# Kernel tuning notes

Measured on AMD Instinct MI355X. Metric: run time of the kernel, lower is better.

## Reference

```python
import jax, jax.numpy as jnp
import numpy as np

INV_SQRT2 = 0.7071067811865476  # ResidualLayer scale in GemNet
SILU_SCALE = 1.0 / 0.6          # ScaledSiLU scale factor


def scaled_silu(x):
    return jax.nn.silu(x) * SILU_SCALE


def setup_inputs() -> dict:
    key = jax.random.key(0)
    ks = jax.random.split(key, 9)
    E, A, D, NB = 200000, 10000, 256, 5  # edges, atoms, emb_size_edge, int_blocks+1

    def w(k, shape):
        fan_in = shape[0]
        return jax.random.normal(k, shape, jnp.float32) * (2.0 / fan_in) ** 0.5

    return {
        "x_cat": jax.random.normal(ks[0], (E, D * NB), jnp.float32),
        "edge_vec": jax.random.normal(ks[1], (E, 3), jnp.float32),
        "edge_idx": jax.random.randint(ks[2], (E,), 0, A),
        "W_in": w(ks[3], (D * NB, D)),
        "W_r1a": w(ks[4], (D, D)),
        "W_r1b": w(ks[5], (D, D)),
        "W_r2a": w(ks[6], (D, D)),
        "W_r2b": w(ks[7], (D, D)),
        "W_out": w(ks[8], (D, 1)),
        "n_atoms": A,
    }


def reference(x_cat, edge_vec, edge_idx, W_in, W_r1a, W_r1b, W_r2a, W_r2b, W_out, n_atoms):
    # out_mlp_F: Dense(in->emb) + 2 residual layers (all Dense are bias-free + ScaledSiLU)
    x = scaled_silu(x_cat @ W_in)                                   # [E, D]
    x = (x + scaled_silu(scaled_silu(x @ W_r1a) @ W_r1b)) * INV_SQRT2
    x = (x + scaled_silu(scaled_silu(x @ W_r2a) @ W_r2b)) * INV_SQRT2
    # out_forces: Dense(D -> 1, bias=False, no activation)
    F_st = x @ W_out                                                # [E, 1]
    # F_st_vec = F_st[:, :, None] * edge_vec[:, None, :] -> squeeze the size-1 dim
    F_vec = F_st * edge_vec                                         # [E, 3]
    # scatter_add over target atom index
    forces = jax.ops.segment_sum(F_vec, edge_idx, num_segments=n_atoms)  # [A, 3]
    return forces
```

## Files before the change

kernel.cpp:

```cpp
#include <hip/hip_runtime.h>

typedef __attribute__((ext_vector_type(4))) float f32x4;
typedef __attribute__((ext_vector_type(8))) __bf16 bf16x8;
typedef __attribute__((ext_vector_type(8))) unsigned short us8;
typedef unsigned short u16;

#define SSILU_SCALE (1.0f / 0.6f)
#define INV_SQRT2 0.70710678118654752f

__device__ __forceinline__ u16 f2bf(float f) {
    __bf16 h = (__bf16)f;
    return __builtin_bit_cast(u16, h);
}
__device__ __forceinline__ float bf2f(u16 h) {
    union { unsigned int u; float f; } v; v.u = ((unsigned int)h) << 16;
    return v.f;
}
__device__ __forceinline__ float ssilu(float x) {
    float e = __expf(-x);
    float s = __builtin_amdgcn_rcpf(1.0f + e);
    return x * s * SSILU_SCALE;
}

__global__ __launch_bounds__(256) void prep_kernel(
    const float* __restrict__ Win, const float* __restrict__ W1a,
    const float* __restrict__ W1b, const float* __restrict__ W2a,
    const float* __restrict__ W2b, u16* __restrict__ WinF,
    u16* __restrict__ Wfrag, float* __restrict__ out, int outN) {
    int i = blockIdx.x * 256 + threadIdx.x;
    if (i < 327680) {
        int e = i & 7, lane = (i >> 3) & 63, n = (i >> 9) & 3;
        int kk = (i >> 11) & 1, w = (i >> 12) & 3, kt = i >> 14;
        int lo = lane & 15, hi = lane >> 4;
        int k = kt * 64 + kk * 32 + hi * 8 + e;
        int col = w * 64 + n * 16 + lo;
        WinF[i] = f2bf(Win[k * 256 + col]);
        return;
    }
    int j = i - 327680;
    if (j < 262144) {
        int g = j >> 16, r = j & 65535;
        int chunk = r >> 9, within = r & 511;
        int lane = within >> 3, e = within & 7;
        int w = chunk >> 5, kk = (chunk >> 2) & 7, n = chunk & 3;
        int lo = lane & 15, hi = lane >> 4;
        int col = w * 64 + n * 16 + lo;
        int k = kk * 32 + hi * 8 + e;
        const float* W = (g == 0) ? W1a : (g == 1) ? W1b : (g == 2) ? W2a : W2b;
        Wfrag[j] = f2bf(W[k * 256 + col]);
        return;
    }
    int z = j - 262144;
    if (z < outN) out[z] = 0.0f;
}

__global__ __launch_bounds__(256, 2) void fused_kernel(
    const float* __restrict__ A, const u16* __restrict__ WinF,
    const u16* __restrict__ Wfrag, const float* __restrict__ Wout,
    const float* __restrict__ evec, const int* __restrict__ eidx,
    float* __restrict__ out) {
    __shared__ u16 xb[64 * 256];
    __shared__ u16 tb[64 * 256];
    __shared__ float fpart[4][64];
    const int t = threadIdx.x, w = t >> 6, l = t & 63;
    const int lo = l & 15, hi = l >> 4;
    const int swz = (lo & 7) << 4;
    const long rowbase = (long)blockIdx.x * 64;
    char* xbB = (char*)xb;
    char* tbB = (char*)tb;
    char* As0 = tbB;
    char* As1 = tbB + 16384;

    f32x4 acc[4][4];
#pragma unroll
    for (int m = 0; m < 4; m++)
#pragma unroll
        for (int n = 0; n < 4; n++) acc[m][n] = (f32x4){0.f, 0.f, 0.f, 0.f};

    float4 va[4][2];
    auto LOADA = [&](int kb) {
#pragma unroll
        for (int c = 0; c < 4; ++c) {
            int idx = t + c * 256;
            int r = idx >> 4, k8 = (idx & 15) * 8;
            const float* s = A + (rowbase + r) * 1280 + kb + k8;
            va[c][0] = *(const float4*)s;
            va[c][1] = *(const float4*)(s + 4);
        }
    };
    auto WRITEA = [&](char* dst) {
#pragma unroll
        for (int c = 0; c < 4; ++c) {
            int idx = t + c * 256;
            int r = idx >> 4, k8 = (idx & 15) * 8;
            us8 p;
            p[0] = f2bf(va[c][0].x); p[1] = f2bf(va[c][0].y);
            p[2] = f2bf(va[c][0].z); p[3] = f2bf(va[c][0].w);
            p[4] = f2bf(va[c][1].x); p[5] = f2bf(va[c][1].y);
            p[6] = f2bf(va[c][1].z); p[7] = f2bf(va[c][1].w);
            *(us8*)(dst + r * 256 + ((k8 * 2) ^ ((r & 7) << 4))) = p;
        }
    };
    const u16* WinFw = WinF + w * 4096 + l * 8;
    auto LOADB = [&](int kt, bf16x8 (&b)[8]) {
        const u16* base = WinFw + kt * 16384;
#pragma unroll
        for (int kkL = 0; kkL < 2; ++kkL)
#pragma unroll
            for (int n = 0; n < 4; ++n)
                b[kkL * 4 + n] = __builtin_bit_cast(bf16x8,
                    *(const us8*)(base + kkL * 2048 + n * 512));
    };
    auto MFMA_HALF = [&](const char* AB, int half, const bf16x8 (&b)[8]) {
#pragma unroll
        for (int kkL = 0; kkL < 2; ++kkL) {
            int kbyte = (half * 2 + kkL) * 64 + hi * 16;
            bf16x8 af[4];
#pragma unroll
            for (int m = 0; m < 4; m++) {
                int r = m * 16 + lo;
                af[m] = __builtin_bit_cast(bf16x8,
                    *(const us8*)(AB + r * 256 + (kbyte ^ swz)));
            }
#pragma unroll
            for (int m = 0; m < 4; m++)
#pragma unroll
                for (int n = 0; n < 4; n++)
                    acc[m][n] = __builtin_amdgcn_mfma_f32_16x16x32_bf16(
                        af[m], b[kkL * 4 + n], acc[m][n], 0, 0, 0);
        }
    };
    auto FENCE = [&]() {
        asm volatile("s_waitcnt lgkmcnt(0)" ::: "memory");
        __builtin_amdgcn_sched_barrier(0);
        __builtin_amdgcn_s_barrier();
    };

    {
        bf16x8 bc[8], bn[8];

        LOADA(0);
        WRITEA(As0);
        LOADB(0, bc);
        LOADA(128);
        FENCE();

        auto STEP = [&](int s, const char* AScur, char* ASnxt) {
            const bool more = (s < 9);
            LOADB(2 * s + 1, bn);
            __builtin_amdgcn_sched_barrier(0);
            MFMA_HALF(AScur, 0, bc);
            if (more) LOADB(2 * s + 2, bc);
            MFMA_HALF(AScur, 1, bn);
            if (more) WRITEA(ASnxt);
            if (s <= 7) LOADA((s + 2) * 128);
            FENCE();
        };

        for (int i = 0; i < 5; ++i) {
            STEP(2 * i,     As0, As1);
            STEP(2 * i + 1, As1, As0);
        }
    }

#pragma unroll
    for (int m = 0; m < 4; m++)
#pragma unroll
        for (int n = 0; n < 4; n++)
#pragma unroll
            for (int j = 0; j < 4; j++) {
                int r = m * 16 + hi * 4 + j;
                int cc = w * 64 + n * 16 + lo;
                *(u16*)(xbB + r * 512 + ((cc * 2) ^ ((r & 7) << 4))) =
                    f2bf(ssilu(acc[m][n][j]));
            }

    const u16* Wfw = Wfrag + w * 16384;
    bf16x8 b0[4], b1[4], b2[4];

    auto LW = [&](const u16* Wg, int kk, bf16x8 (&b)[4]) {
        const u16* base = Wg + kk * 2048 + l * 8;
#pragma unroll
        for (int n = 0; n < 4; ++n)
            b[n] = __builtin_bit_cast(bf16x8, *(const us8*)(base + n * 512));
    };
    auto GEMM = [&](const char* AB, const u16* Wg) {
#pragma unroll
        for (int m = 0; m < 4; m++)
#pragma unroll
            for (int n = 0; n < 4; n++) acc[m][n] = (f32x4){0.f, 0.f, 0.f, 0.f};
#pragma unroll
        for (int kk = 0; kk < 8; ++kk) {
            if (kk < 6) {
                const int s = (kk + 2) % 3;
                if (s == 0)      LW(Wg, kk + 2, b0);
                else if (s == 1) LW(Wg, kk + 2, b1);
                else             LW(Wg, kk + 2, b2);
            }
            int kbyte = kk * 64 + hi * 16;
            bf16x8 af[4];
#pragma unroll
            for (int m = 0; m < 4; m++) {
                int r = m * 16 + lo;
                af[m] = __builtin_bit_cast(bf16x8,
                    *(const us8*)(AB + r * 512 + (kbyte ^ ((r & 7) << 4))));
            }
            const bf16x8 (&bu)[4] = (kk % 3 == 0) ? b0 : (kk % 3 == 1) ? b1 : b2;
#pragma unroll
            for (int m = 0; m < 4; m++)
#pragma unroll
                for (int n = 0; n < 4; n++)
                    acc[m][n] = __builtin_amdgcn_mfma_f32_16x16x32_bf16(
                        af[m], bu[n], acc[m][n], 0, 0, 0);
        }
    };

    LW(Wfw + 0 * 65536, 0, b0);
    LW(Wfw + 0 * 65536, 1, b1);
    FENCE();
    GEMM(xbB, Wfw + 0 * 65536);
#pragma unroll
    for (int m = 0; m < 4; m++)
#pragma unroll
        for (int n = 0; n < 4; n++)
#pragma unroll
            for (int j = 0; j < 4; j++) {
                int r = m * 16 + hi * 4 + j;
                int cc = w * 64 + n * 16 + lo;
                *(u16*)(tbB + r * 512 + ((cc * 2) ^ ((r & 7) << 4))) =
                    f2bf(ssilu(acc[m][n][j]));
            }
    LW(Wfw + 1 * 65536, 0, b0);
    LW(Wfw + 1 * 65536, 1, b1);
    FENCE();

    GEMM(tbB, Wfw + 1 * 65536);
#pragma unroll
    for (int m = 0; m < 4; m++)
#pragma unroll
        for (int n = 0; n < 4; n++)
#pragma unroll
            for (int j = 0; j < 4; j++) {
                int r = m * 16 + hi * 4 + j;
                int cc = w * 64 + n * 16 + lo;
                char* p = xbB + r * 512 + ((cc * 2) ^ ((r & 7) << 4));
                float xn = (bf2f(*(u16*)p) + ssilu(acc[m][n][j])) * INV_SQRT2;
                *(u16*)p = f2bf(xn);
            }
    LW(Wfw + 2 * 65536, 0, b0);
    LW(Wfw + 2 * 65536, 1, b1);
    FENCE();

    GEMM(xbB, Wfw + 2 * 65536);
#pragma unroll
    for (int m = 0; m < 4; m++)
#pragma unroll
        for (int n = 0; n < 4; n++)
#pragma unroll
            for (int j = 0; j < 4; j++) {
                int r = m * 16 + hi * 4 + j;
                int cc = w * 64 + n * 16 + lo;
                *(u16*)(tbB + r * 512 + ((cc * 2) ^ ((r & 7) << 4))) =
                    f2bf(ssilu(acc[m][n][j]));
            }
    LW(Wfw + 3 * 65536, 0, b0);
    LW(Wfw + 3 * 65536, 1, b1);
    FENCE();

    GEMM(tbB, Wfw + 3 * 65536);
    float wo[4];
#pragma unroll
    for (int n = 0; n < 4; n++) wo[n] = Wout[w * 64 + n * 16 + lo];

    float part[4][4];
#pragma unroll
    for (int m = 0; m < 4; m++)
#pragma unroll
        for (int j = 0; j < 4; j++) part[m][j] = 0.f;
#pragma unroll
    for (int m = 0; m < 4; m++)
#pragma unroll
        for (int n = 0; n < 4; n++)
#pragma unroll
            for (int j = 0; j < 4; j++) {
                int r = m * 16 + hi * 4 + j;
                int cc = w * 64 + n * 16 + lo;
                const char* p = xbB + r * 512 + ((cc * 2) ^ ((r & 7) << 4));
                float xf = (bf2f(*(const u16*)p) + ssilu(acc[m][n][j])) * INV_SQRT2;
                part[m][j] += xf * wo[n];
            }
#pragma unroll
    for (int m = 0; m < 4; m++)
#pragma unroll
        for (int j = 0; j < 4; j++) {
            float v = part[m][j];
            v += __shfl_xor(v, 1);
            v += __shfl_xor(v, 2);
            v += __shfl_xor(v, 4);
            v += __shfl_xor(v, 8);
            if (lo == 0) fpart[w][m * 16 + hi * 4 + j] = v;
        }
    __syncthreads();

    if (t < 64) {
        int r = t;
        float F = fpart[0][r] + fpart[1][r] + fpart[2][r] + fpart[3][r];
        long e = rowbase + r;
        float vx = evec[e * 3 + 0], vy = evec[e * 3 + 1], vz = evec[e * 3 + 2];
        int a = eidx[e];
        atomicAdd(&out[a * 3 + 0], F * vx);
        atomicAdd(&out[a * 3 + 1], F * vy);
        atomicAdd(&out[a * 3 + 2], F * vz);
    }
}

extern "C" void kernel_launch(void* const* d_in, const int* in_sizes, int n_in,
                              void* d_out, int out_size, void* d_ws, size_t ws_size,
                              hipStream_t stream) {
    const float* x_cat = (const float*)d_in[0];
    const float* evec  = (const float*)d_in[1];
    const int*   eidx  = (const int*)d_in[2];
    const float* Win   = (const float*)d_in[3];
    const float* W1a   = (const float*)d_in[4];
    const float* W1b   = (const float*)d_in[5];
    const float* W2a   = (const float*)d_in[6];
    const float* W2b   = (const float*)d_in[7];
    const float* Wout  = (const float*)d_in[8];
    float* out = (float*)d_out;
    const int E = in_sizes[1] / 3;

    u16* WinF  = (u16*)d_ws;
    u16* Wfrag = WinF + 327680;

    int prepN = 327680 + 262144 + out_size;
    prep_kernel<<<(prepN + 255) / 256, 256, 0, stream>>>(
        Win, W1a, W1b, W2a, W2b, WinF, Wfrag, out, out_size);
    fused_kernel<<<E / 64, 256, 0, stream>>>(
        x_cat, WinF, Wfrag, Wout, evec, eidx, out);
}
```

Baseline: 383.8 us.

## Warp-specialize fused MLP into persistent producer/consumer blocks

Replaces the one-tile-per-block kernel with a persistent grid of 256 blocks of 512 threads. Half the threads run the input GEMM (x_cat @ W_in) for tile s into a double-buffered activation buffer, while the other half run the four residual GEMMs and the scatter for tile s-1. The two roles stay in lockstep by issuing matching barrier counts. The goal is to overlap the bandwidth-bound input streaming with the compute-bound residual MLP. In exchange, each role gets half the waves, the A staging tile shrinks to K=64, and correctness depends on the barrier counts matching exactly.

```diff
diff --git a/kernel.cpp b/kernel.cpp
--- a/kernel.cpp
+++ b/kernel.cpp
@@ -54,263 +54,277 @@
     if (z < outN) out[z] = 0.0f;
 }
 
-__global__ __launch_bounds__(256, 2) void fused_kernel(
+__global__ __launch_bounds__(512, 1) void fused_pc(
     const float* __restrict__ A, const u16* __restrict__ WinF,
     const u16* __restrict__ Wfrag, const float* __restrict__ Wout,
     const float* __restrict__ evec, const int* __restrict__ eidx,
-    float* __restrict__ out) {
-    __shared__ u16 xb[64 * 256];
+    float* __restrict__ out, int ntiles) {
+    __shared__ u16 xb[2][64 * 256];
+    __shared__ u16 As[2][64 * 64];
     __shared__ u16 tb[64 * 256];
     __shared__ float fpart[4][64];
-    const int t = threadIdx.x, w = t >> 6, l = t & 63;
+    const int tid = threadIdx.x;
+    const int role = __builtin_amdgcn_readfirstlane(tid >> 8);
+    const int t = tid & 255;
+    const int w = t >> 6, l = t & 63;
     const int lo = l & 15, hi = l >> 4;
     const int swz = (lo & 7) << 4;
-    const long rowbase = (long)blockIdx.x * 64;
-    char* xbB = (char*)xb;
-    char* tbB = (char*)tb;
-    char* As0 = tbB;
-    char* As1 = tbB + 16384;
-
-    f32x4 acc[4][4];
-#pragma unroll
-    for (int m = 0; m < 4; m++)
-#pragma unroll
-        for (int n = 0; n < 4; n++) acc[m][n] = (f32x4){0.f, 0.f, 0.f, 0.f};
-
-    float4 va[4][2];
-    auto LOADA = [&](int kb) {
-#pragma unroll
-        for (int c = 0; c < 4; ++c) {
-            int idx = t + c * 256;
-            int r = idx >> 4, k8 = (idx & 15) * 8;
-            const float* s = A + (rowbase + r) * 1280 + kb + k8;
-            va[c][0] = *(const float4*)s;
-            va[c][1] = *(const float4*)(s + 4);
-        }
-    };
-    auto WRITEA = [&](char* dst) {
-#pragma unroll
-        for (int c = 0; c < 4; ++c) {
-            int idx = t + c * 256;
-            int r = idx >> 4, k8 = (idx & 15) * 8;
-            us8 p;
-            p[0] = f2bf(va[c][0].x); p[1] = f2bf(va[c][0].y);
-            p[2] = f2bf(va[c][0].z); p[3] = f2bf(va[c][0].w);
-            p[4] = f2bf(va[c][1].x); p[5] = f2bf(va[c][1].y);
-            p[6] = f2bf(va[c][1].z); p[7] = f2bf(va[c][1].w);
-            *(us8*)(dst + r * 256 + ((k8 * 2) ^ ((r & 7) << 4))) = p;
-        }
-    };
-    const u16* WinFw = WinF + w * 4096 + l * 8;
-    auto LOADB = [&](int kt, bf16x8 (&b)[8]) {
-        const u16* base = WinFw + kt * 16384;
-#pragma unroll
-        for (int kkL = 0; kkL < 2; ++kkL)
-#pragma unroll
-            for (int n = 0; n < 4; ++n)
-                b[kkL * 4 + n] = __builtin_bit_cast(bf16x8,
-                    *(const us8*)(base + kkL * 2048 + n * 512));
-    };
-    auto MFMA_HALF = [&](const char* AB, int half, const bf16x8 (&b)[8]) {
-#pragma unroll
-        for (int kkL = 0; kkL < 2; ++kkL) {
-            int kbyte = (half * 2 + kkL) * 64 + hi * 16;
-            bf16x8 af[4];
-#pragma unroll
-            for (int m = 0; m < 4; m++) {
-                int r = m * 16 + lo;
-                af[m] = __builtin_bit_cast(bf16x8,
-                    *(const us8*)(AB + r * 256 + (kbyte ^ swz)));
-            }
-#pragma unroll
-            for (int m = 0; m < 4; m++)
-#pragma unroll
-                for (int n = 0; n < 4; n++)
-                    acc[m][n] = __builtin_amdgcn_mfma_f32_16x16x32_bf16(
-                        af[m], b[kkL * 4 + n], acc[m][n], 0, 0, 0);
-        }
-    };
-    auto FENCE = [&]() {
+    const int bid = blockIdx.x;
+    const int NT = (ntiles - bid + 255) / 256;
+
+    auto BAR = []() { __builtin_amdgcn_s_barrier(); };
+    auto FENCE = []() {
         asm volatile("s_waitcnt lgkmcnt(0)" ::: "memory");
         __builtin_amdgcn_sched_barrier(0);
         __builtin_amdgcn_s_barrier();
     };
 
-    {
-        bf16x8 bc[8], bn[8];
-
-        LOADA(0);
-        WRITEA(As0);
-        LOADB(0, bc);
-        LOADA(128);
-        FENCE();
-
-        auto STEP = [&](int s, const char* AScur, char* ASnxt) {
-            const bool more = (s < 9);
-            LOADB(2 * s + 1, bn);
-            __builtin_amdgcn_sched_barrier(0);
-            MFMA_HALF(AScur, 0, bc);
-            if (more) LOADB(2 * s + 2, bc);
-            MFMA_HALF(AScur, 1, bn);
-            if (more) WRITEA(ASnxt);
-            if (s <= 7) LOADA((s + 2) * 128);
-            FENCE();
-        };
-
-        for (int i = 0; i < 5; ++i) {
-            STEP(2 * i,     As0, As1);
-            STEP(2 * i + 1, As1, As0);
+    if (role == 0) {
+        char* As0 = (char*)As[0];
+        char* As1 = (char*)As[1];
+        const u16* WinFw = WinF + w * 4096 + l * 8;
+        for (int s = 0; s <= NT; ++s) {
+            if (s >= NT) {
+                for (int k = 0; k < 22; ++k) BAR();
+                continue;
+            }
+            const long rowbase = (long)(bid + 256 * s) * 64;
+            char* xbp = (char*)xb[s & 1];
+
+            f32x4 acc[4][4];
+#pragma unroll
+            for (int m = 0; m < 4; m++)
+#pragma unroll
+                for (int n = 0; n < 4; n++) acc[m][n] = (f32x4){0.f, 0.f, 0.f, 0.f};
+
+            float4 va[2][2];
+            auto LOADA = [&](int kb) {
+#pragma unroll
+                for (int c = 0; c < 2; ++c) {
+                    int idx = t + c * 256;
+                    int r = idx >> 3, k8 = (idx & 7) * 8;
+                    const float* sp = A + (rowbase + r) * 1280 + kb + k8;
+                    va[c][0] = *(const float4*)sp;
+                    va[c][1] = *(const float4*)(sp + 4);
+                }
+            };
+            auto WRITEA = [&](char* dst) {
+#pragma unroll
+                for (int c = 0; c < 2; ++c) {
+                    int idx = t + c * 256;
+                    int r = idx >> 3, k8 = (idx & 7) * 8;
+                    us8 p;
+                    p[0] = f2bf(va[c][0].x); p[1] = f2bf(va[c][0].y);
+                    p[2] = f2bf(va[c][0].z); p[3] = f2bf(va[c][0].w);
+                    p[4] = f2bf(va[c][1].x); p[5] = f2bf(va[c][1].y);
+                    p[6] = f2bf(va[c][1].z); p[7] = f2bf(va[c][1].w);
+                    *(us8*)(dst + r * 128 + ((k8 * 2) ^ ((r & 7) << 4))) = p;
+                }
+            };
+            auto LOADB = [&](int kt, int kk, bf16x8 (&b)[4]) {
+                const u16* base = WinFw + kt * 16384 + kk * 2048;
+#pragma unroll
+                for (int n = 0; n < 4; ++n)
+                    b[n] = __builtin_bit_cast(bf16x8, *(const us8*)(base + n * 512));
+            };
+            auto MFMA_KK = [&](const char* AB, int kk, const bf16x8 (&bc)[4]) {
+                int kbyte = kk * 64 + hi * 16;
+                bf16x8 af[4];
+#pragma unroll
+                for (int m = 0; m < 4; m++) {
+                    int r = m * 16 + lo;
+                    af[m] = __builtin_bit_cast(bf16x8,
+                        *(const us8*)(AB + r * 128 + (kbyte ^ swz)));
+                }
+#pragma unroll
+                for (int m = 0; m < 4; m++)
+#pragma unroll
+                    for (int n = 0; n < 4; n++)
+                        acc[m][n] = __builtin_amdgcn_mfma_f32_16x16x32_bf16(
+                            af[m], bc[n], acc[m][n], 0, 0, 0);
+            };
+
+            bf16x8 bc[4], bn[4];
+            LOADA(0);
+            WRITEA(As0);
+            LOADB(0, 0, bc);
+            LOADA(64);
+            FENCE();
+            for (int kt = 0; kt < 20; ++kt) {
+                const char* AScur = (kt & 1) ? As1 : As0;
+                char* ASnxt = (kt & 1) ? As0 : As1;
+                const bool more = (kt < 19);
+                LOADB(kt, 1, bn);
+                MFMA_KK(AScur, 0, bc);
+                if (more) LOADB(kt + 1, 0, bc);
+                MFMA_KK(AScur, 1, bn);
+                if (more) WRITEA(ASnxt);
+                if (kt <= 17) LOADA((kt + 2) * 64);
+                FENCE();
+            }
+#pragma unroll
+            for (int m = 0; m < 4; m++)
+#pragma unroll
+                for (int n = 0; n < 4; n++)
+#pragma unroll
+                    for (int j = 0; j < 4; j++) {
+                        int r = m * 16 + hi * 4 + j;
+                        int cc = w * 64 + n * 16 + lo;
+                        *(u16*)(xbp + r * 512 + ((cc * 2) ^ ((r & 7) << 4))) =
+                            f2bf(ssilu(acc[m][n][j]));
+                    }
+            FENCE();
         }
-    }
-
-#pragma unroll
-    for (int m = 0; m < 4; m++)
-#pragma unroll
-        for (int n = 0; n < 4; n++)
-#pragma unroll
-            for (int j = 0; j < 4; j++) {
-                int r = m * 16 + hi * 4 + j;
-                int cc = w * 64 + n * 16 + lo;
-                *(u16*)(xbB + r * 512 + ((cc * 2) ^ ((r & 7) << 4))) =
-                    f2bf(ssilu(acc[m][n][j]));
+    } else {
+        char* tbB = (char*)tb;
+        const u16* Wfw = Wfrag + w * 16384;
+        float wo[4];
+#pragma unroll
+        for (int n = 0; n < 4; n++) wo[n] = Wout[w * 64 + n * 16 + lo];
+
+        for (int s = 0; s <= NT; ++s) {
+            if (s == 0) {
+                for (int k = 0; k < 22; ++k) BAR();
+                continue;
             }
-
-    const u16* Wfw = Wfrag + w * 16384;
-    bf16x8 b0[4], b1[4], b2[4];
-
-    auto LW = [&](const u16* Wg, int kk, bf16x8 (&b)[4]) {
-        const u16* base = Wg + kk * 2048 + l * 8;
-#pragma unroll
-        for (int n = 0; n < 4; ++n)
-            b[n] = __builtin_bit_cast(bf16x8, *(const us8*)(base + n * 512));
-    };
-    auto GEMM = [&](const char* AB, const u16* Wg) {
-#pragma unroll
-        for (int m = 0; m < 4; m++)
-#pragma unroll
-            for (int n = 0; n < 4; n++) acc[m][n] = (f32x4){0.f, 0.f, 0.f, 0.f};
-#pragma unroll
-        for (int kk = 0; kk < 8; ++kk) {
-            if (kk < 6) {
-                const int s = (kk + 2) % 3;
-                if (s == 0)      LW(Wg, kk + 2, b0);
-                else if (s == 1) LW(Wg, kk + 2, b1);
-                else             LW(Wg, kk + 2, b2);
+            const long rowbase = (long)(bid + 256 * (s - 1)) * 64;
+            char* xbp = (char*)xb[(s - 1) & 1];
+
+            f32x4 acc[4][4];
+            bf16x8 b0[4], b1[4], b2[4];
+            auto LW = [&](const u16* Wg, int kk, bf16x8 (&b)[4]) {
+                const u16* base = Wg + kk * 2048 + l * 8;
+#pragma unroll
+                for (int n = 0; n < 4; ++n)
+                    b[n] = __builtin_bit_cast(bf16x8, *(const us8*)(base + n * 512));
+            };
+            auto GEMM = [&](const char* AB, const u16* Wg) {
+#pragma unroll
+                for (int m = 0; m < 4; m++)
+#pragma unroll
+                    for (int n = 0; n < 4; n++) acc[m][n] = (f32x4){0.f, 0.f, 0.f, 0.f};
+#pragma unroll
+                for (int kk = 0; kk < 8; ++kk) {
+                    if (kk < 6) {
+                        const int st = (kk + 2) % 3;
+                        if (st == 0)      LW(Wg, kk + 2, b0);
+                        else if (st == 1) LW(Wg, kk + 2, b1);
+                        else              LW(Wg, kk + 2, b2);
+                    }
+                    int kbyte = kk * 64 + hi * 16;
+                    bf16x8 af[4];
+#pragma unroll
+                    for (int m = 0; m < 4; m++) {
+                        int r = m * 16 + lo;
+                        af[m] = __builtin_bit_cast(bf16x8,
+                            *(const us8*)(AB + r * 512 + (kbyte ^ ((r & 7) << 4))));
+                    }
+                    const bf16x8 (&bu)[4] = (kk % 3 == 0) ? b0 : (kk % 3 == 1) ? b1 : b2;
+#pragma unroll
+                    for (int m = 0; m < 4; m++)
+#pragma unroll
+                        for (int n = 0; n < 4; n++)
+                            acc[m][n] = __builtin_amdgcn_mfma_f32_16x16x32_bf16(
+                                af[m], bu[n], acc[m][n], 0, 0, 0);
+                }
+            };
+
+            LW(Wfw + 0 * 65536, 0, b0);
+            LW(Wfw + 0 * 65536, 1, b1);
+            BAR();
+
+            GEMM(xbp, Wfw + 0 * 65536);
+#pragma unroll
+            for (int m = 0; m < 4; m++)
+#pragma unroll
+                for (int n = 0; n < 4; n++)
+#pragma unroll
+                    for (int j = 0; j < 4; j++) {
+                        int r = m * 16 + hi * 4 + j;
+                        int cc = w * 64 + n * 16 + lo;
+                        *(u16*)(tbB + r * 512 + ((cc * 2) ^ ((r & 7) << 4))) =
+                            f2bf(ssilu(acc[m][n][j]));
+                    }
+            LW(Wfw + 1 * 65536, 0, b0);
+            LW(Wfw + 1 * 65536, 1, b1);
+            FENCE();
+
+            GEMM(tbB, Wfw + 1 * 65536);
+#pragma unroll
+            for (int m = 0; m < 4; m++)
+#pragma unroll
+                for (int n = 0; n < 4; n++)
+#pragma unroll
+                    for (int j = 0; j < 4; j++) {
+                        int r = m * 16 + hi * 4 + j;
+                        int cc = w * 64 + n * 16 + lo;
+                        char* p = xbp + r * 512 + ((cc * 2) ^ ((r & 7) << 4));
+                        float xn = (bf2f(*(u16*)p) + ssilu(acc[m][n][j])) * INV_SQRT2;
+                        *(u16*)p = f2bf(xn);
+                    }
+            LW(Wfw + 2 * 65536, 0, b0);
+            LW(Wfw + 2 * 65536, 1, b1);
+            FENCE();
+
+            GEMM(xbp, Wfw + 2 * 65536);
+#pragma unroll
+            for (int m = 0; m < 4; m++)
+#pragma unroll
+                for (int n = 0; n < 4; n++)
+#pragma unroll
+                    for (int j = 0; j < 4; j++) {
+                        int r = m * 16 + hi * 4 + j;
+                        int cc = w * 64 + n * 16 + lo;
+                        *(u16*)(tbB + r * 512 + ((cc * 2) ^ ((r & 7) << 4))) =
+                            f2bf(ssilu(acc[m][n][j]));
+                    }
+            LW(Wfw + 3 * 65536, 0, b0);
+            LW(Wfw + 3 * 65536, 1, b1);
+            FENCE();
+
+            GEMM(tbB, Wfw + 3 * 65536);
+            float part[4][4];
+#pragma unroll
+            for (int m = 0; m < 4; m++)
+#pragma unroll
+                for (int j = 0; j < 4; j++) part[m][j] = 0.f;
+#pragma unroll
+            for (int m = 0; m < 4; m++)
+#pragma unroll
+                for (int n = 0; n < 4; n++)
+#pragma unroll
+                    for (int j = 0; j < 4; j++) {
+                        int r = m * 16 + hi * 4 + j;
+                        int cc = w * 64 + n * 16 + lo;
+                        const char* p = xbp + r * 512 + ((cc * 2) ^ ((r & 7) << 4));
+                        float xf = (bf2f(*(const u16*)p) + ssilu(acc[m][n][j])) * INV_SQRT2;
+                        part[m][j] += xf * wo[n];
+                    }
+#pragma unroll
+            for (int m = 0; m < 4; m++)
+#pragma unroll
+                for (int j = 0; j < 4; j++) {
+                    float v = part[m][j];
+                    v += __shfl_xor(v, 1);
+                    v += __shfl_xor(v, 2);
+                    v += __shfl_xor(v, 4);
+                    v += __shfl_xor(v, 8);
+                    if (lo == 0) fpart[w][m * 16 + hi * 4 + j] = v;
+                }
+            FENCE();
+
+            if (t < 64) {
+                int r = t;
+                float F = fpart[0][r] + fpart[1][r] + fpart[2][r] + fpart[3][r];
+                long e = rowbase + r;
+                float vx = evec[e * 3 + 0], vy = evec[e * 3 + 1], vz = evec[e * 3 + 2];
+                int a = eidx[e];
+                atomicAdd(&out[a * 3 + 0], F * vx);
+                atomicAdd(&out[a * 3 + 1], F * vy);
+                atomicAdd(&out[a * 3 + 2], F * vz);
             }
-            int kbyte = kk * 64 + hi * 16;
-            bf16x8 af[4];
-#pragma unroll
-            for (int m = 0; m < 4; m++) {
-                int r = m * 16 + lo;
-                af[m] = __builtin_bit_cast(bf16x8,
-                    *(const us8*)(AB + r * 512 + (kbyte ^ ((r & 7) << 4))));
-            }
-            const bf16x8 (&bu)[4] = (kk % 3 == 0) ? b0 : (kk % 3 == 1) ? b1 : b2;
-#pragma unroll
-            for (int m = 0; m < 4; m++)
-#pragma unroll
-                for (int n = 0; n < 4; n++)
-                    acc[m][n] = __builtin_amdgcn_mfma_f32_16x16x32_bf16(
-                        af[m], bu[n], acc[m][n], 0, 0, 0);
+            for (int k = 0; k < 17; ++k) BAR();
         }
-    };
-
-    LW(Wfw + 0 * 65536, 0, b0);
-    LW(Wfw + 0 * 65536, 1, b1);
-    FENCE();
-    GEMM(xbB, Wfw + 0 * 65536);
-#pragma unroll
-    for (int m = 0; m < 4; m++)
-#pragma unroll
-        for (int n = 0; n < 4; n++)
-#pragma unroll
-            for (int j = 0; j < 4; j++) {
-                int r = m * 16 + hi * 4 + j;
-                int cc = w * 64 + n * 16 + lo;
-                *(u16*)(tbB + r * 512 + ((cc * 2) ^ ((r & 7) << 4))) =
-                    f2bf(ssilu(acc[m][n][j]));
-            }
-    LW(Wfw + 1 * 65536, 0, b0);
-    LW(Wfw + 1 * 65536, 1, b1);
-    FENCE();
-
-    GEMM(tbB, Wfw + 1 * 65536);
-#pragma unroll
-    for (int m = 0; m < 4; m++)
-#pragma unroll
-        for (int n = 0; n < 4; n++)
-#pragma unroll
-            for (int j = 0; j < 4; j++) {
-                int r = m * 16 + hi * 4 + j;
-                int cc = w * 64 + n * 16 + lo;
-                char* p = xbB + r * 512 + ((cc * 2) ^ ((r & 7) << 4));
-                float xn = (bf2f(*(u16*)p) + ssilu(acc[m][n][j])) * INV_SQRT2;
-                *(u16*)p = f2bf(xn);
-            }
-    LW(Wfw + 2 * 65536, 0, b0);
-    LW(Wfw + 2 * 65536, 1, b1);
-    FENCE();
-
-    GEMM(xbB, Wfw + 2 * 65536);
-#pragma unroll
-    for (int m = 0; m < 4; m++)
-#pragma unroll
-        for (int n = 0; n < 4; n++)
-#pragma unroll
-            for (int j = 0; j < 4; j++) {
-                int r = m * 16 + hi * 4 + j;
-                int cc = w * 64 + n * 16 + lo;
-                *(u16*)(tbB + r * 512 + ((cc * 2) ^ ((r & 7) << 4))) =
-                    f2bf(ssilu(acc[m][n][j]));
-            }
-    LW(Wfw + 3 * 65536, 0, b0);
-    LW(Wfw + 3 * 65536, 1, b1);
-    FENCE();
-
-    GEMM(tbB, Wfw + 3 * 65536);
-    float wo[4];
-#pragma unroll
-    for (int n = 0; n < 4; n++) wo[n] = Wout[w * 64 + n * 16 + lo];
-
-    float part[4][4];
-#pragma unroll
-    for (int m = 0; m < 4; m++)
-#pragma unroll
-        for (int j = 0; j < 4; j++) part[m][j] = 0.f;
-#pragma unroll
-    for (int m = 0; m < 4; m++)
-#pragma unroll
-        for (int n = 0; n < 4; n++)
-#pragma unroll
-            for (int j = 0; j < 4; j++) {
-                int r = m * 16 + hi * 4 + j;
-                int cc = w * 64 + n * 16 + lo;
-                const char* p = xbB + r * 512 + ((cc * 2) ^ ((r & 7) << 4));
-                float xf = (bf2f(*(const u16*)p) + ssilu(acc[m][n][j])) * INV_SQRT2;
-                part[m][j] += xf * wo[n];
-            }
-#pragma unroll
-    for (int m = 0; m < 4; m++)
-#pragma unroll
-        for (int j = 0; j < 4; j++) {
-            float v = part[m][j];
-            v += __shfl_xor(v, 1);
-            v += __shfl_xor(v, 2);
-            v += __shfl_xor(v, 4);
-            v += __shfl_xor(v, 8);
-            if (lo == 0) fpart[w][m * 16 + hi * 4 + j] = v;
-        }
-    __syncthreads();
-
-    if (t < 64) {
-        int r = t;
-        float F = fpart[0][r] + fpart[1][r] + fpart[2][r] + fpart[3][r];
-        long e = rowbase + r;
-        float vx = evec[e * 3 + 0], vy = evec[e * 3 + 1], vz = evec[e * 3 + 2];
-        int a = eidx[e];
-        atomicAdd(&out[a * 3 + 0], F * vx);
-        atomicAdd(&out[a * 3 + 1], F * vy);
-        atomicAdd(&out[a * 3 + 2], F * vz);
     }
 }
 
@@ -328,6 +342,7 @@
     const float* Wout  = (const float*)d_in[8];
     float* out = (float*)d_out;
     const int E = in_sizes[1] / 3;
+    const int ntiles = E / 64;
 
     u16* WinF  = (u16*)d_ws;
     u16* Wfrag = WinF + 327680;
@@ -335,6 +350,6 @@
     int prepN = 327680 + 262144 + out_size;
     prep_kernel<<<(prepN + 255) / 256, 256, 0, stream>>>(
         Win, W1a, W1b, W2a, W2b, WinF, Wfrag, out, out_size);
-    fused_kernel<<<E / 64, 256, 0, stream>>>(
-        x_cat, WinF, Wfrag, Wout, evec, eidx, out);
-}
+    fused_pc<<<256, 512, 0, stream>>>(
+        x_cat, WinF, Wfrag, Wout, evec, eidx, out, ntiles);
+}
```

Result: slower. 747.2 us (+94.7%).
